# Optimization experiments

Measured on AMD Instinct MI355X. Metric: run time of the kernel, lower is better.

Reference implementation:

```python
import jax, jax.numpy as jnp
import numpy as np

B, H, T, DH = 4, 8, 4096, 128
BUCKETS = 32


def setup_inputs() -> dict:
    key = jax.random.key(0)
    k1, k2, k3, k4 = jax.random.split(key, 4)
    q = jax.random.normal(k1, (B, H, T, DH), jnp.float32)
    k = jax.random.normal(k2, (B, H, T, DH), jnp.float32)
    v = jax.random.normal(k3, (B, H, T, DH), jnp.float32)
    W_sort = jax.random.normal(k4, (1, H, 2 * DH, BUCKETS), jnp.float32)
    return {"q": q, "k": k, "v": v, "W_sort": W_sort}


def _build_mask(h, buckets, bsz):
    hh = h // 2
    i = jnp.arange(bsz)[:, None]
    j = jnp.arange(2 * bsz)[None, :]
    # reordered-bucket half (j < bsz) fully visible; current bucket causal
    causal = (j < bsz) | (i >= (j - bsz))  # [bsz, 2*bsz]
    # rotated heads, last bucket: rows > 0 cannot see first bsz+1 cols; row 0 can
    special = (j <= bsz) & (i > 0)
    last_rot = causal & ~special
    mask = jnp.broadcast_to(causal, (h, buckets, bsz, 2 * bsz))
    mask = mask.at[hh:, -1].set(last_rot)
    return mask  # [h, buckets, bsz, 2*bsz] bool


def reference(q, k, v, W_sort):
    b, h, t, d_h = q.shape
    buckets = W_sort.shape[-1]
    d = h * d_h  # full model dim, used for the attention scale
    bsz = t // buckets
    hh = h // 2

    def rot(x, n):
        # rotate only the second half of heads along time
        return jnp.concatenate([x[:, :hh], jnp.roll(x[:, hh:], n, axis=2)], axis=1)

    q = rot(q, -(bsz - 1))
    k = rot(k, -(bsz - 1))
    v = rot(v, -(bsz - 1))

    bq = q.reshape(b, h, buckets, bsz, d_h)
    bk = k.reshape(b, h, buckets, bsz, d_h)
    bv = v.reshape(b, h, buckets, bsz, d_h)

    # --- sort net: cumulative-average key features of first token per bucket ---
    r = jnp.arange(1, t + 1, dtype=k.dtype)
    kc = jnp.cumsum(k, axis=2) / r[None, None, :, None]
    kr = jnp.concatenate([kc, k], axis=-1).reshape(b, h, buckets, bsz, 2 * d_h)
    x = kr[:, :, :, 0]  # [b, h, buckets, 2*d_h]
    R = jax.nn.leaky_relu(jnp.einsum('bhue,hev->bhuv', x, W_sort[0]))
    R = jax.nn.softmax(R, axis=-1)
    R = jnp.tril(R, -1)
    # keep only the top-1 entry per row (first argmax, like torch.topk k=1)
    idx = jnp.argmax(R, axis=-1)
    R = jnp.max(R, axis=-1, keepdims=True) * jax.nn.one_hot(idx, buckets, dtype=R.dtype)

    # --- permutation gather of one past bucket of k/v per query bucket ---
    k_re = jnp.einsum('bhuv,bhvtd->bhutd', R, bk)
    v_re = jnp.einsum('bhuv,bhvtd->bhutd', R, bv)
    bk2 = jnp.concatenate([k_re, bk], axis=3)  # [b,h,buckets,2*bsz,d_h]
    bv2 = jnp.concatenate([v_re, bv], axis=3)

    dots = jnp.einsum('bhuie,bhuje->bhuij', bq, bk2) * (float(d) ** -0.5)
    mask = _build_mask(h, buckets, bsz)
    neg = -jnp.finfo(dots.dtype).max
    dots = jnp.where(mask[None], dots, neg)
    attn = jax.nn.softmax(dots, axis=-1)
    out = jnp.einsum('bhuij,bhuje->bhuie', attn, bv2)
    out = out.reshape(b, h, t, d_h)
    out = rot(out, bsz - 1)
    return out
```

## Files before the change

kernel.cpp:

```cpp
#include <hip/hip_runtime.h>

constexpr int T_    = 4096;
constexpr int DH_   = 128;
constexpr int NB_   = 32;
constexpr int BSZ_  = 128;
constexpr int HH_   = 4;
constexpr int H_    = 8;
constexpr int BH_   = 32;

typedef __attribute__((ext_vector_type(8))) short short8;
typedef __attribute__((ext_vector_type(4))) float f32x4;

__device__ __forceinline__ unsigned short f2bf(float f) {
  unsigned int u = __float_as_uint(f);
  unsigned int r = (u + 0x7FFFu + ((u >> 16) & 1u)) >> 16;
  return (unsigned short)r;
}

__global__ __launch_bounds__(256)
void k_bucket_sums(const float* __restrict__ k,
                   float* __restrict__ bucketsum,
                   float* __restrict__ firstrow) {
  __shared__ float4 red[8][32];
  int blk = blockIdx.x;
  int u = blk & (NB_ - 1);
  int bh = blk >> 5;
  int h = bh & (H_ - 1);
  bool rot = (h >= HH_);
  int tid = threadIdx.x;
  int rq = tid >> 5;
  int l  = tid & 31;
  int d0 = l * 4;
  const float* kb = k + (size_t)bh * T_ * DH_;

  float4 s = {0.f, 0.f, 0.f, 0.f};
  float4 first = {0.f, 0.f, 0.f, 0.f};
  #pragma unroll
  for (int it = 0; it < 16; ++it) {
    int i = it * 8 + rq;
    int t = u * BSZ_ + i;
    if (rot) t = (t + (BSZ_ - 1)) & (T_ - 1);
    float4 a = *(const float4*)(kb + (size_t)t * DH_ + d0);
    s.x += a.x; s.y += a.y; s.z += a.z; s.w += a.w;
    if (it == 0 && rq == 0) first = a;
  }
  red[rq][l] = s;
  __syncthreads();
  if (rq == 0) {
    float4 acc = {0.f, 0.f, 0.f, 0.f};
    #pragma unroll
    for (int j = 0; j < 8; ++j) {
      float4 a = red[j][l];
      acc.x += a.x; acc.y += a.y; acc.z += a.z; acc.w += a.w;
    }
    *(float4*)(bucketsum + (size_t)blk * DH_ + d0) = acc;
    *(float4*)(firstrow  + (size_t)blk * DH_ + d0) = first;
  }
}

__global__ __launch_bounds__(256)
void k_routing(const float* __restrict__ W,
               const float* __restrict__ bucketsum,
               const float* __restrict__ firstrow,
               float* __restrict__ scaleArr,
               int* __restrict__ idxArr) {
  __shared__ float Wl[2 * DH_ * NB_];
  __shared__ float Xl[NB_][2 * DH_ + 1];
  __shared__ float Rl[NB_][36];
  int bh = blockIdx.x;
  int h = bh & (H_ - 1);
  int tid = threadIdx.x;

  const float4* Wg = (const float4*)(W + (size_t)h * 2 * DH_ * NB_);
  #pragma unroll
  for (int rep = 0; rep < 8; ++rep)
    ((float4*)Wl)[tid + rep * 256] = Wg[tid + rep * 256];

  if (tid < DH_) {
    int d = tid;
    float S = 0.f;
    for (int u = 0; u < NB_; ++u) {
      float fr = firstrow [((size_t)bh * NB_ + u) * DH_ + d];
      float bs = bucketsum[((size_t)bh * NB_ + u) * DH_ + d];
      Xl[u][d]        = (S + fr) / (float)(u * BSZ_ + 1);
      Xl[u][DH_ + d]  = fr;
      S += bs;
    }
  }
  __syncthreads();

  {
    int u = tid >> 3;
    int vg = tid & 7;
    float4 racc = {0.f, 0.f, 0.f, 0.f};
    for (int e = 0; e < 2 * DH_; ++e) {
      float xv = Xl[u][e];
      float4 wv = *(const float4*)(Wl + e * NB_ + vg * 4);
      racc.x += xv * wv.x; racc.y += xv * wv.y;
      racc.z += xv * wv.z; racc.w += xv * wv.w;
    }
    racc.x = (racc.x > 0.f) ? racc.x : 0.01f * racc.x;
    racc.y = (racc.y > 0.f) ? racc.y : 0.01f * racc.y;
    racc.z = (racc.z > 0.f) ? racc.z : 0.01f * racc.z;
    racc.w = (racc.w > 0.f) ? racc.w : 0.01f * racc.w;
    *(float4*)(&Rl[u][vg * 4]) = racc;
  }
  __syncthreads();

  if (tid < NB_) {
    int u = tid;
    float m = -3.4e38f;
    float r[NB_];
    #pragma unroll
    for (int v = 0; v < NB_; ++v) { r[v] = Rl[u][v]; m = fmaxf(m, r[v]); }
    float Z = 0.f;
    #pragma unroll
    for (int v = 0; v < NB_; ++v) Z += expf(r[v] - m);
    float best = -3.4e38f; int bi = 0;
    for (int v = 0; v < u; ++v) {
      if (r[v] > best) { best = r[v]; bi = v; }
    }
    float sc = (u == 0) ? 0.f : expf(best - m) / Z;
    scaleArr[bh * NB_ + u] = sc;
    idxArr  [bh * NB_ + u] = (u == 0) ? 0 : bi;
  }
}

__global__ __launch_bounds__(512, 4)
void k_attn(const float* __restrict__ q, const float* __restrict__ k,
            const float* __restrict__ v, const float* __restrict__ scaleArr,
            const int* __restrict__ idxArr, float* __restrict__ out) {
  __shared__ unsigned short RA[128 * 128];
  __shared__ unsigned short RB[128 * 128];

  int blk0 = blockIdx.x;
  int blk  = ((blk0 & 7) << 7) | (blk0 >> 3);
  int u  = blk & (NB_ - 1);
  int bh = blk >> 5;
  int h  = bh & (H_ - 1);
  bool rot = (h >= HH_);
  float sc = scaleArr[bh * NB_ + u];
  int  src = idxArr  [bh * NB_ + u];
  const size_t base = (size_t)bh * T_ * DH_;

  int tid  = threadIdx.x;
  int lane = tid & 63;
  int w    = tid >> 6;
  int g    = lane >> 4;
  int c    = lane & 15;

  short8 qf[4];
  {
    int t = u * BSZ_ + 16 * w + c;
    if (rot) t = (t + (BSZ_ - 1)) & (T_ - 1);
    const float* qrow = q + base + (size_t)t * DH_;
    #pragma unroll
    for (int kt = 0; kt < 4; ++kt) {
      int d0 = kt * 32 + g * 8;
      float4 a = *(const float4*)(qrow + d0);
      float4 b = *(const float4*)(qrow + d0 + 4);
      short8 f;
      f[0] = (short)f2bf(a.x); f[1] = (short)f2bf(a.y);
      f[2] = (short)f2bf(a.z); f[3] = (short)f2bf(a.w);
      f[4] = (short)f2bf(b.x); f[5] = (short)f2bf(b.y);
      f[6] = (short)f2bf(b.z); f[7] = (short)f2bf(b.w);
      qf[kt] = f;
    }
  }

  #pragma unroll
  for (int rep = 0; rep < 16; ++rep) {
    int chunk = tid + rep * 512;
    int jr = chunk >> 5;
    int c0 = (chunk & 31) * 4;
    int t; float mul; unsigned short* Rg;
    if (jr < BSZ_) { t = src * BSZ_ + jr;         mul = sc;  Rg = RA; }
    else           { t = u  * BSZ_ + (jr - BSZ_); mul = 1.f; Rg = RB; }
    if (rot) t = (t + (BSZ_ - 1)) & (T_ - 1);
    float4 a = *(const float4*)(k + base + (size_t)t * DH_ + c0);
    ushort4 wv;
    wv.x = f2bf(a.x * mul); wv.y = f2bf(a.y * mul);
    wv.z = f2bf(a.z * mul); wv.w = f2bf(a.w * mul);
    int row = jr & 127;
    *(ushort4*)((char*)Rg + row * 256 + ((c0 * 2) ^ ((row & 15) << 4))) = wv;
  }
  __syncthreads();

  f32x4 acc[16];
  #pragma unroll
  for (int jt = 0; jt < 16; ++jt) acc[jt] = f32x4{0.f, 0.f, 0.f, 0.f};

  __builtin_amdgcn_s_setprio(1);
  #pragma unroll
  for (int kt = 0; kt < 4; ++kt) {
    #pragma unroll
    for (int jt = 0; jt < 16; ++jt) {
      const unsigned short* Rg = (jt < 8) ? RA : RB;
      int row = (jt & 7) * 16 + c;
      short8 bfr = *(const short8*)((const char*)Rg + row * 256 + ((kt * 64 + g * 16) ^ (c << 4)));
      acc[jt] = __builtin_amdgcn_mfma_f32_16x16x32_bf16(qf[kt], bfr, acc[jt], 0, 0, 0);
    }
  }
  __builtin_amdgcn_s_setprio(0);

  __syncthreads();

  const bool lastrot = rot && (u == NB_ - 1);
  #pragma unroll
  for (int r = 0; r < 4; ++r) {
    int i = 16 * w + 4 * g + r;
    float mx = -3.4e38f;
    #pragma unroll
    for (int jt = 0; jt < 16; ++jt) {
      int j = jt * 16 + c;
      float s = acc[jt][r] * 0.03125f;
      bool causal = (j < BSZ_) || (i >= j - BSZ_);
      bool vis = lastrot ? (causal && !((j <= BSZ_) && (i > 0))) : causal;
      s = vis ? s : -3.4e38f;
      acc[jt][r] = s;
      mx = fmaxf(mx, s);
    }
    mx = fmaxf(mx, __shfl_xor(mx, 1));
    mx = fmaxf(mx, __shfl_xor(mx, 2));
    mx = fmaxf(mx, __shfl_xor(mx, 4));
    mx = fmaxf(mx, __shfl_xor(mx, 8));
    float zs = 0.f;
    #pragma unroll
    for (int jt = 0; jt < 16; ++jt) {
      float p = expf(acc[jt][r] - mx);
      acc[jt][r] = p;
      zs += p;
    }
    zs += __shfl_xor(zs, 1);
    zs += __shfl_xor(zs, 2);
    zs += __shfl_xor(zs, 4);
    zs += __shfl_xor(zs, 8);
    float rz = 1.f / zs;
    #pragma unroll
    for (int jt = 0; jt < 16; ++jt) acc[jt][r] *= rz;
    #pragma unroll
    for (int jt = 0; jt < 8; ++jt) {
      int jc = jt * 16 + c;
      *(unsigned short*)((char*)RA + i * 256 + ((jc * 2) ^ ((i & 15) << 4))) = f2bf(acc[jt][r]);
    }
  }

  auto stageVT = [&](int sb, float mul) {
    #pragma unroll
    for (int rep = 0; rep < 2; ++rep) {
      int chunk = tid + rep * 512;
      int dt = chunk & 31, j4 = chunk >> 5;
      int d0 = dt * 4, j0 = j4 * 4;
      float rr[4][4];
      #pragma unroll
      for (int jj = 0; jj < 4; ++jj) {
        int t = sb * BSZ_ + j0 + jj;
        if (rot) t = (t + (BSZ_ - 1)) & (T_ - 1);
        float4 a = *(const float4*)(v + base + (size_t)t * DH_ + d0);
        rr[jj][0] = a.x * mul; rr[jj][1] = a.y * mul;
        rr[jj][2] = a.z * mul; rr[jj][3] = a.w * mul;
      }
      #pragma unroll
      for (int m = 0; m < 4; ++m) {
        ushort4 wv;
        wv.x = f2bf(rr[0][m]); wv.y = f2bf(rr[1][m]);
        wv.z = f2bf(rr[2][m]); wv.w = f2bf(rr[3][m]);
        int row = d0 + m;
        *(ushort4*)((char*)RB + row * 256 + ((j0 * 2) ^ ((row & 15) << 4))) = wv;
      }
    }
  };
  stageVT(src, sc);
  __syncthreads();

  f32x4 o[8];
  #pragma unroll
  for (int nt = 0; nt < 8; ++nt) o[nt] = f32x4{0.f, 0.f, 0.f, 0.f};

  auto pv = [&]() {
    __builtin_amdgcn_s_setprio(1);
    #pragma unroll
    for (int kt = 0; kt < 4; ++kt) {
      int prow = 16 * w + c;
      short8 pa = *(const short8*)((const char*)RA + prow * 256 + ((kt * 64 + g * 16) ^ (c << 4)));
      #pragma unroll
      for (int nt = 0; nt < 8; ++nt) {
        int vrow = nt * 16 + c;
        short8 vb = *(const short8*)((const char*)RB + vrow * 256 + ((kt * 64 + g * 16) ^ (c << 4)));
        o[nt] = __builtin_amdgcn_mfma_f32_16x16x32_bf16(pa, vb, o[nt], 0, 0, 0);
      }
    }
    __builtin_amdgcn_s_setprio(0);
  };
  pv();

  __syncthreads();

  #pragma unroll
  for (int r = 0; r < 4; ++r) {
    int i = 16 * w + 4 * g + r;
    #pragma unroll
    for (int jt = 8; jt < 16; ++jt) {
      int jc = (jt - 8) * 16 + c;
      *(unsigned short*)((char*)RA + i * 256 + ((jc * 2) ^ ((i & 15) << 4))) = f2bf(acc[jt][r]);
    }
  }
  stageVT(u, 1.f);
  __syncthreads();

  pv();

  #pragma unroll
  for (int r = 0; r < 4; ++r) {
    int il = 4 * g + r;
    int t = u * BSZ_ + 16 * w + il;
    if (rot) t = (t + (BSZ_ - 1)) & (T_ - 1);
    float* orow = out + base + (size_t)t * DH_;
    #pragma unroll
    for (int nt = 0; nt < 8; ++nt) {
      orow[nt * 16 + c] = o[nt][r];
    }
  }
}

extern "C" void kernel_launch(void* const* d_in, const int* in_sizes, int n_in,
                              void* d_out, int out_size, void* d_ws, size_t ws_size,
                              hipStream_t stream) {
  const float* q = (const float*)d_in[0];
  const float* k = (const float*)d_in[1];
  const float* v = (const float*)d_in[2];
  const float* W = (const float*)d_in[3];
  float* out = (float*)d_out;

  float* bucketsum = (float*)d_ws;
  float* firstrow  = bucketsum + 131072;
  float* scaleArr  = firstrow + 131072;
  int*   idxArr    = (int*)(scaleArr + 1024);

  k_bucket_sums<<<BH_ * NB_, 256, 0, stream>>>(k, bucketsum, firstrow);
  k_routing<<<BH_, 256, 0, stream>>>(W, bucketsum, firstrow, scaleArr, idxArr);
  k_attn<<<BH_ * NB_, 512, 0, stream>>>(q, k, v, scaleArr, idxArr, out);
}
```

Baseline: 92.09 us.

## Split V staging into quarters and overlap V loads with QK and softmax

Restructures the attention kernel so V is loaded from global memory in four 64-row quarters, prefetched into registers before and during QK^T and softmax, and written into a third LDS buffer. This hides the V load latency and removes some barriers. The routing scale is now folded into the softmax scale and the P write instead of into K/V, exp2f replaces expf, and scale/index are packed into one float2 load. It uses more LDS (16KB extra) and more registers, which may lower occupancy, and the chunked PV uses 64-column swizzled tiles.

```diff
diff --git a/kernel.cpp b/kernel.cpp
--- a/kernel.cpp
+++ b/kernel.cpp
@@ -62,8 +62,7 @@
 void k_routing(const float* __restrict__ W,
                const float* __restrict__ bucketsum,
                const float* __restrict__ firstrow,
-               float* __restrict__ scaleArr,
-               int* __restrict__ idxArr) {
+               float2* __restrict__ scIdx) {
   __shared__ float Wl[2 * DH_ * NB_];
   __shared__ float Xl[NB_][2 * DH_ + 1];
   __shared__ float Rl[NB_][36];
@@ -121,17 +120,18 @@
       if (r[v] > best) { best = r[v]; bi = v; }
     }
     float sc = (u == 0) ? 0.f : expf(best - m) / Z;
-    scaleArr[bh * NB_ + u] = sc;
-    idxArr  [bh * NB_ + u] = (u == 0) ? 0 : bi;
+    int  idx = (u == 0) ? 0 : bi;
+    scIdx[bh * NB_ + u] = make_float2(sc, __int_as_float(idx));
   }
 }
 
 __global__ __launch_bounds__(512, 4)
 void k_attn(const float* __restrict__ q, const float* __restrict__ k,
-            const float* __restrict__ v, const float* __restrict__ scaleArr,
-            const int* __restrict__ idxArr, float* __restrict__ out) {
-  __shared__ unsigned short RA[128 * 128];
-  __shared__ unsigned short RB[128 * 128];
+            const float* __restrict__ v, const float2* __restrict__ scIdx,
+            float* __restrict__ out) {
+  __shared__ __align__(16) unsigned short L0[128 * 128];
+  __shared__ __align__(16) unsigned short L1[128 * 128];
+  __shared__ __align__(16) unsigned short L2[64 * 128];
 
   int blk0 = blockIdx.x;
   int blk  = ((blk0 & 7) << 7) | (blk0 >> 3);
@@ -139,8 +139,9 @@
   int bh = blk >> 5;
   int h  = bh & (H_ - 1);
   bool rot = (h >= HH_);
-  float sc = scaleArr[bh * NB_ + u];
-  int  src = idxArr  [bh * NB_ + u];
+  float2 si = scIdx[bh * NB_ + u];
+  float sc = si.x;
+  int  src = __float_as_int(si.y);
   const size_t base = (size_t)bh * T_ * DH_;
 
   int tid  = threadIdx.x;
@@ -156,14 +157,11 @@
     const float* qrow = q + base + (size_t)t * DH_;
     #pragma unroll
     for (int kt = 0; kt < 4; ++kt) {
-      int d0 = kt * 32 + g * 8;
-      float4 a = *(const float4*)(qrow + d0);
-      float4 b = *(const float4*)(qrow + d0 + 4);
+      f32x4 a = *(const f32x4*)(qrow + kt * 32 + g * 8);
+      f32x4 b = *(const f32x4*)(qrow + kt * 32 + g * 8 + 4);
       short8 f;
-      f[0] = (short)f2bf(a.x); f[1] = (short)f2bf(a.y);
-      f[2] = (short)f2bf(a.z); f[3] = (short)f2bf(a.w);
-      f[4] = (short)f2bf(b.x); f[5] = (short)f2bf(b.y);
-      f[6] = (short)f2bf(b.z); f[7] = (short)f2bf(b.w);
+      f[0]=(short)f2bf(a[0]); f[1]=(short)f2bf(a[1]); f[2]=(short)f2bf(a[2]); f[3]=(short)f2bf(a[3]);
+      f[4]=(short)f2bf(b[0]); f[5]=(short)f2bf(b[1]); f[6]=(short)f2bf(b[2]); f[7]=(short)f2bf(b[3]);
       qf[kt] = f;
     }
   }
@@ -173,31 +171,56 @@
     int chunk = tid + rep * 512;
     int jr = chunk >> 5;
     int c0 = (chunk & 31) * 4;
-    int t; float mul; unsigned short* Rg;
-    if (jr < BSZ_) { t = src * BSZ_ + jr;         mul = sc;  Rg = RA; }
-    else           { t = u  * BSZ_ + (jr - BSZ_); mul = 1.f; Rg = RB; }
+    int t = (jr < BSZ_) ? (src * BSZ_ + jr) : (u * BSZ_ + (jr - BSZ_));
     if (rot) t = (t + (BSZ_ - 1)) & (T_ - 1);
-    float4 a = *(const float4*)(k + base + (size_t)t * DH_ + c0);
+    f32x4 a = *(const f32x4*)(k + base + (size_t)t * DH_ + c0);
     ushort4 wv;
-    wv.x = f2bf(a.x * mul); wv.y = f2bf(a.y * mul);
-    wv.z = f2bf(a.z * mul); wv.w = f2bf(a.w * mul);
+    wv.x=f2bf(a[0]); wv.y=f2bf(a[1]); wv.z=f2bf(a[2]); wv.w=f2bf(a[3]);
+    unsigned short* Rg = (jr < BSZ_) ? L0 : L1;
     int row = jr & 127;
     *(ushort4*)((char*)Rg + row * 256 + ((c0 * 2) ^ ((row & 15) << 4))) = wv;
   }
+
+  int vdt = tid & 31, vj4 = tid >> 5;
+  int vd0 = vdt * 4, vjl0 = vj4 * 4;
+
+  auto vt_load = [&](int qtr, f32x4* rr) {
+    #pragma unroll
+    for (int jj = 0; jj < 4; ++jj) {
+      int jgl = qtr * 64 + vjl0 + jj;
+      int t = (jgl < BSZ_) ? (src * BSZ_ + jgl) : (u * BSZ_ + (jgl - BSZ_));
+      if (rot) t = (t + (BSZ_ - 1)) & (T_ - 1);
+      rr[jj] = *(const f32x4*)(v + base + (size_t)t * DH_ + vd0);
+    }
+  };
+  auto vt_write = [&](const f32x4* rr, unsigned short* Rg) {
+    #pragma unroll
+    for (int m = 0; m < 4; ++m) {
+      ushort4 wv;
+      wv.x=f2bf(rr[0][m]); wv.y=f2bf(rr[1][m]); wv.z=f2bf(rr[2][m]); wv.w=f2bf(rr[3][m]);
+      int row = vd0 + m;
+      *(ushort4*)((char*)Rg + row * 128 + ((vjl0 * 2) ^ ((row & 7) << 4))) = wv;
+    }
+  };
+
+  f32x4 rr0[4];
+  vt_load(0, rr0); vt_write(rr0, L2);
+  f32x4 rq1[4];
+  vt_load(1, rq1);
+
   __syncthreads();
 
   f32x4 acc[16];
   #pragma unroll
   for (int jt = 0; jt < 16; ++jt) acc[jt] = f32x4{0.f, 0.f, 0.f, 0.f};
-
   __builtin_amdgcn_s_setprio(1);
   #pragma unroll
   for (int kt = 0; kt < 4; ++kt) {
     #pragma unroll
     for (int jt = 0; jt < 16; ++jt) {
-      const unsigned short* Rg = (jt < 8) ? RA : RB;
+      const unsigned short* Rg = (jt < 8) ? L0 : L1;
       int row = (jt & 7) * 16 + c;
-      short8 bfr = *(const short8*)((const char*)Rg + row * 256 + ((kt * 64 + g * 16) ^ (c << 4)));
+      short8 bfr = *(const short8*)((const char*)Rg + row * 256 + ((kt * 64 + g * 16) ^ ((row & 15) << 4)));
       acc[jt] = __builtin_amdgcn_mfma_f32_16x16x32_bf16(qf[kt], bfr, acc[jt], 0, 0, 0);
     }
   }
@@ -205,7 +228,18 @@
 
   __syncthreads();
 
+  vt_write(rq1, L1);
+  {
+    f32x4 rq2[4];
+    vt_load(2, rq2); vt_write(rq2, L1 + 64 * 128);
+  }
+  f32x4 rq3[4];
+  vt_load(3, rq3);
+
   const bool lastrot = rot && (u == NB_ - 1);
+  const float LOG2E = 1.44269504f;
+  float scale1 = 0.03125f * LOG2E * sc;
+  float scale2 = 0.03125f * LOG2E;
   #pragma unroll
   for (int r = 0; r < 4; ++r) {
     int i = 16 * w + 4 * g + r;
@@ -213,7 +247,7 @@
     #pragma unroll
     for (int jt = 0; jt < 16; ++jt) {
       int j = jt * 16 + c;
-      float s = acc[jt][r] * 0.03125f;
+      float s = acc[jt][r] * ((jt < 8) ? scale1 : scale2);
       bool causal = (j < BSZ_) || (i >= j - BSZ_);
       bool vis = lastrot ? (causal && !((j <= BSZ_) && (i > 0))) : causal;
       s = vis ? s : -3.4e38f;
@@ -227,7 +261,7 @@
     float zs = 0.f;
     #pragma unroll
     for (int jt = 0; jt < 16; ++jt) {
-      float p = expf(acc[jt][r] - mx);
+      float p = exp2f(acc[jt][r] - mx);
       acc[jt][r] = p;
       zs += p;
     }
@@ -236,79 +270,68 @@
     zs += __shfl_xor(zs, 4);
     zs += __shfl_xor(zs, 8);
     float rz = 1.f / zs;
-    #pragma unroll
-    for (int jt = 0; jt < 16; ++jt) acc[jt][r] *= rz;
-    #pragma unroll
-    for (int jt = 0; jt < 8; ++jt) {
-      int jc = jt * 16 + c;
-      *(unsigned short*)((char*)RA + i * 256 + ((jc * 2) ^ ((i & 15) << 4))) = f2bf(acc[jt][r]);
-    }
-  }
-
-  auto stageVT = [&](int sb, float mul) {
-    #pragma unroll
-    for (int rep = 0; rep < 2; ++rep) {
-      int chunk = tid + rep * 512;
-      int dt = chunk & 31, j4 = chunk >> 5;
-      int d0 = dt * 4, j0 = j4 * 4;
-      float rr[4][4];
-      #pragma unroll
-      for (int jj = 0; jj < 4; ++jj) {
-        int t = sb * BSZ_ + j0 + jj;
-        if (rot) t = (t + (BSZ_ - 1)) & (T_ - 1);
-        float4 a = *(const float4*)(v + base + (size_t)t * DH_ + d0);
-        rr[jj][0] = a.x * mul; rr[jj][1] = a.y * mul;
-        rr[jj][2] = a.z * mul; rr[jj][3] = a.w * mul;
-      }
-      #pragma unroll
-      for (int m = 0; m < 4; ++m) {
-        ushort4 wv;
-        wv.x = f2bf(rr[0][m]); wv.y = f2bf(rr[1][m]);
-        wv.z = f2bf(rr[2][m]); wv.w = f2bf(rr[3][m]);
-        int row = d0 + m;
-        *(ushort4*)((char*)RB + row * 256 + ((j0 * 2) ^ ((row & 15) << 4))) = wv;
-      }
-    }
-  };
-  stageVT(src, sc);
-  __syncthreads();
+    float rzs = rz * sc;
+    #pragma unroll
+    for (int jt = 0; jt < 4; ++jt) {
+      int jl = jt * 16 + c;
+      *(unsigned short*)((char*)L0 + i * 128 + ((jl * 2) ^ ((i & 7) << 4))) = f2bf(acc[jt][r] * rzs);
+    }
+    #pragma unroll
+    for (int jt = 4; jt < 8; ++jt) {
+      int jl = (jt - 4) * 16 + c;
+      *(unsigned short*)((char*)(L0 + 64 * 128) + i * 128 + ((jl * 2) ^ ((i & 7) << 4))) = f2bf(acc[jt][r] * rzs);
+    }
+    #pragma unroll
+    for (int jt = 8; jt < 16; ++jt) acc[jt][r] *= rz;
+  }
 
   f32x4 o[8];
   #pragma unroll
   for (int nt = 0; nt < 8; ++nt) o[nt] = f32x4{0.f, 0.f, 0.f, 0.f};
 
-  auto pv = [&]() {
+  auto pv = [&](const unsigned short* P, const unsigned short* V) {
     __builtin_amdgcn_s_setprio(1);
     #pragma unroll
-    for (int kt = 0; kt < 4; ++kt) {
+    for (int ktq = 0; ktq < 2; ++ktq) {
       int prow = 16 * w + c;
-      short8 pa = *(const short8*)((const char*)RA + prow * 256 + ((kt * 64 + g * 16) ^ (c << 4)));
+      short8 pa = *(const short8*)((const char*)P + prow * 128 + ((ktq * 64 + g * 16) ^ ((prow & 7) << 4)));
       #pragma unroll
       for (int nt = 0; nt < 8; ++nt) {
         int vrow = nt * 16 + c;
-        short8 vb = *(const short8*)((const char*)RB + vrow * 256 + ((kt * 64 + g * 16) ^ (c << 4)));
+        short8 vb = *(const short8*)((const char*)V + vrow * 128 + ((ktq * 64 + g * 16) ^ ((vrow & 7) << 4)));
         o[nt] = __builtin_amdgcn_mfma_f32_16x16x32_bf16(pa, vb, o[nt], 0, 0, 0);
       }
     }
     __builtin_amdgcn_s_setprio(0);
   };
-  pv();
-
-  __syncthreads();
+
+  pv(L0, L2);
+  __syncthreads();
+  vt_write(rq3, L2);
+  pv(L0 + 64 * 128, L1);
 
   #pragma unroll
   for (int r = 0; r < 4; ++r) {
     int i = 16 * w + 4 * g + r;
     #pragma unroll
-    for (int jt = 8; jt < 16; ++jt) {
-      int jc = (jt - 8) * 16 + c;
-      *(unsigned short*)((char*)RA + i * 256 + ((jc * 2) ^ ((i & 15) << 4))) = f2bf(acc[jt][r]);
-    }
-  }
-  stageVT(u, 1.f);
-  __syncthreads();
-
-  pv();
+    for (int jt = 8; jt < 12; ++jt) {
+      int jl = (jt - 8) * 16 + c;
+      *(unsigned short*)((char*)L0 + i * 128 + ((jl * 2) ^ ((i & 7) << 4))) = f2bf(acc[jt][r]);
+    }
+  }
+  pv(L0, L1 + 64 * 128);
+
+  #pragma unroll
+  for (int r = 0; r < 4; ++r) {
+    int i = 16 * w + 4 * g + r;
+    #pragma unroll
+    for (int jt = 12; jt < 16; ++jt) {
+      int jl = (jt - 12) * 16 + c;
+      *(unsigned short*)((char*)(L0 + 64 * 128) + i * 128 + ((jl * 2) ^ ((i & 7) << 4))) = f2bf(acc[jt][r]);
+    }
+  }
+  __syncthreads();
+  pv(L0 + 64 * 128, L2);
 
   #pragma unroll
   for (int r = 0; r < 4; ++r) {
@@ -332,12 +355,11 @@
   const float* W = (const float*)d_in[3];
   float* out = (float*)d_out;
 
-  float* bucketsum = (float*)d_ws;
-  float* firstrow  = bucketsum + 131072;
-  float* scaleArr  = firstrow + 131072;
-  int*   idxArr    = (int*)(scaleArr + 1024);
+  float*  bucketsum = (float*)d_ws;
+  float*  firstrow  = bucketsum + 131072;
+  float2* scIdx     = (float2*)(firstrow + 131072);
 
   k_bucket_sums<<<BH_ * NB_, 256, 0, stream>>>(k, bucketsum, firstrow);
-  k_routing<<<BH_, 256, 0, stream>>>(W, bucketsum, firstrow, scaleArr, idxArr);
-  k_attn<<<BH_ * NB_, 512, 0, stream>>>(q, k, v, scaleArr, idxArr, out);
-}
+  k_routing<<<BH_, 256, 0, stream>>>(W, bucketsum, firstrow, scIdx);
+  k_attn<<<BH_ * NB_, 512, 0, stream>>>(q, k, v, scIdx, out);
+}
```

Measured after the change: 122.4 us. 33.0% more time.
